# Performance work log

Hardware: AMD Instinct MI355X
Metric: run time of the kernel (lower is better)

Reference implementation:

```python
import jax, jax.numpy as jnp
import numpy as np

B, T_DEC, U, T_K, D, V = 32, 64, 32, 64, 512, 50257


def setup_inputs() -> dict:
    key = jax.random.key(0)
    ks = jax.random.split(key, 24)
    s = 0.02  # weight init scale
    inp = {
        "target_features": jax.random.normal(ks[0], (B, T_DEC, D), jnp.float32),
        "target_mask": jnp.ones((B, T_DEC), jnp.float32),
        "encode_features": jax.random.normal(ks[1], (B, U, D), jnp.float32),
        "utterance_mask": jnp.ones((B, U), jnp.float32),
        "token_features": jax.random.normal(ks[2], (U, B, T_K, D), jnp.float32),
        "token_mask": jnp.ones((U, B, T_K), jnp.float32),
        "coverage": jnp.zeros((B, U), jnp.float32),
        "token_coverage": jnp.zeros((U, B, T_K), jnp.float32),
        # utterance_attention params
        "ua_Wp": jax.random.normal(ks[3], (D, D), jnp.float32) * s,
        "ua_bp": jnp.zeros((D,), jnp.float32),
        "ua_v": jax.random.normal(ks[4], (D,), jnp.float32) * s,
        "ua_wc": jax.random.normal(ks[5], (D,), jnp.float32) * s,  # W_c: Linear(1,D) weight, squeezed
        # token_attention params
        "ta_Wp": jax.random.normal(ks[6], (D, D), jnp.float32) * s,
        "ta_bp": jnp.zeros((D,), jnp.float32),
        "ta_v": jax.random.normal(ks[7], (D,), jnp.float32) * s,
        "ta_wc": jax.random.normal(ks[8], (D,), jnp.float32) * s,
        # pointer-gen + output projections
        "pgen_W": jax.random.normal(ks[9], (1, 2 * D), jnp.float32) * s,
        "pgen_b": jnp.zeros((1,), jnp.float32),
        "out1_W": jax.random.normal(ks[10], (D, 2 * D), jnp.float32) * s,
        "out1_b": jnp.zeros((D,), jnp.float32),
        "out2_W": jax.random.normal(ks[11], (V, D), jnp.float32) * s,
        "out2_b": jnp.zeros((V,), jnp.float32),
        # LayerNorm params
        "ln_g": jnp.ones((D,), jnp.float32),
        "ln_b": jnp.zeros((D,), jnp.float32),
    }
    return inp


def _local_attn(t, enc, mask, cov, Wp, bp, v, wc):
    # t: [..., D] decoder state, enc: [..., T, D], mask/cov: [..., T]
    dec = t @ Wp.T + bp                                   # [..., D]
    att = enc + dec[..., None, :] + cov[..., None] * wc   # additive + coverage feature
    scores = jnp.einsum('...td,d->...t', jnp.tanh(att), v)
    attn_ = jax.nn.softmax(scores, axis=-1) * mask
    nf = attn_.sum(-1, keepdims=True)
    attn = attn_ / jnp.where(nf == 0, 1.0, nf)
    out = jnp.einsum('...t,...td->...d', attn, enc)       # context vector
    return out, attn, cov + attn


def reference(target_features, target_mask, encode_features, utterance_mask,
              token_features, token_mask, coverage, token_coverage,
              ua_Wp, ua_bp, ua_v, ua_wc, ta_Wp, ta_bp, ta_v, ta_wc,
              pgen_W, pgen_b, out1_W, out1_b, out2_W, out2_b, ln_g, ln_b):
    # layers == [] so the transformer-layer loop is a no-op; then LayerNorm.
    mu = target_features.mean(-1, keepdims=True)
    var = ((target_features - mu) ** 2).mean(-1, keepdims=True)
    normed = (target_features - mu) * jax.lax.rsqrt(var + 1e-5) * ln_g + ln_b
    local_dec = normed[:, -1, :]                           # [B, D]

    # utterance-level attention
    u_out, u_attn, u_cov = _local_attn(local_dec, encode_features, utterance_mask,
                                       coverage, ua_Wp, ua_bp, ua_v, ua_wc)

    # per-utterance token attention, batched over U (replaces Python for-loop)
    tok = jax.vmap(lambda e, m, c: _local_attn(local_dec, e, m, c, ta_Wp, ta_bp, ta_v, ta_wc))
    utters_out, utters_attn, next_tok_cov = tok(token_features, token_mask, token_coverage)
    # utters_out: [U, B, D], utters_attn/next_tok_cov: [U, B, T_K]

    p_gen = jax.nn.sigmoid(jnp.concatenate([u_out, local_dec], axis=1) @ pgen_W.T + pgen_b)

    # topk(k=1) == argmax (first max on ties, matching torch.topk)
    utter_index = jnp.argmax(u_attn, axis=1)               # [B]
    idx = jnp.arange(u_attn.shape[0])
    target_attn_dist = utters_attn[utter_index, idx, :]    # [B, T_K]
    target_out = utters_out[utter_index, idx, :]           # [B, D]

    h = jnp.concatenate([target_out, local_dec], axis=1) @ out1_W.T + out1_b
    logits = h @ out2_W.T + out2_b
    vocab_dist = jax.nn.softmax(logits, axis=1)
    return vocab_dist, target_attn_dist, p_gen, u_cov, next_tok_cov, utter_index
```

## Files before the change

### kernel.cpp

```cpp
#include <hip/hip_runtime.h>
#include <math.h>

#define BB 32
#define TDEC 64
#define UU 32
#define TK 64
#define DD 512
#define VV 50257
#define NT5 3142
#define K5_GRID 1024

#define WS_LDEC   0
#define WS_DEC_U  16384
#define WS_DEC_T  32768
#define WS_UATTN  49152
#define WS_UIDX   50176
#define WS_TSC    50208
#define WS_TATTN  115744
#define WS_TOUT   181280
#define WS_H      197664
#define WS_PSUM   214048
#define WS_SUMS   246816

#define OUT_VOCAB 0
#define OUT_TAD   1608224
#define OUT_PGEN  1610272
#define OUT_UCOV  1610304
#define OUT_NTC   1611328
#define OUT_UIDX  1676864

__device__ __forceinline__ float wave_sum(float v) {
    #pragma unroll
    for (int off = 32; off > 0; off >>= 1) v += __shfl_xor(v, off, 64);
    return v;
}
__device__ __forceinline__ float wave_max(float v) {
    #pragma unroll
    for (int off = 32; off > 0; off >>= 1) v = fmaxf(v, __shfl_xor(v, off, 64));
    return v;
}
__device__ __forceinline__ float fast_tanh(float x) {
    float e2 = __expf(2.0f * x);
    return 1.0f - 2.0f * __builtin_amdgcn_rcpf(e2 + 1.0f);
}

__global__ __launch_bounds__(256) void k1_ln_proj(
    const float* __restrict__ tf, const float* __restrict__ ln_g, const float* __restrict__ ln_b,
    const float* __restrict__ ua_Wp, const float* __restrict__ ua_bp,
    const float* __restrict__ ta_Wp, const float* __restrict__ ta_bp,
    float* __restrict__ ws)
{
    int b = blockIdx.x >> 3, slice = blockIdx.x & 7;
    int tid = threadIdx.x, wid = tid >> 6, lane = tid & 63;
    __shared__ __align__(16) float ldec[DD];
    __shared__ float red[4];
    const float* x = tf + ((size_t)b * TDEC + (TDEC - 1)) * DD;
    float x0 = x[tid], x1 = x[tid + 256];

    float s = wave_sum(x0 + x1);
    if (lane == 0) red[wid] = s;
    __syncthreads();
    float mean = (red[0] + red[1] + red[2] + red[3]) * (1.0f / DD);
    __syncthreads();
    float d0 = x0 - mean, d1 = x1 - mean;
    s = wave_sum(d0 * d0 + d1 * d1);
    if (lane == 0) red[wid] = s;
    __syncthreads();
    float var = (red[0] + red[1] + red[2] + red[3]) * (1.0f / DD);
    float inv = rsqrtf(var + 1e-5f);
    float n0 = d0 * inv * ln_g[tid] + ln_b[tid];
    float n1 = d1 * inv * ln_g[tid + 256] + ln_b[tid + 256];
    ldec[tid] = n0; ldec[tid + 256] = n1;
    if (slice == 0) {
        ws[WS_LDEC + b * DD + tid] = n0;
        ws[WS_LDEC + b * DD + tid + 256] = n1;
    }
    __syncthreads();

    int r = slice * 128 + (tid >> 1);
    int m = r >> 9, rr = r & 511;
    int kh = tid & 1;
    const float* Wp = m ? ta_Wp : ua_Wp;
    const float* bp = m ? ta_bp : ua_bp;
    const float4* wr = (const float4*)(Wp + (size_t)rr * DD + kh * 256);
    const float4* hl = (const float4*)ldec + kh * 64;
    float acc = 0.f;
    #pragma unroll 8
    for (int i = 0; i < 64; i++) {
        float4 w = wr[i]; float4 h = hl[i];
        acc += w.x * h.x + w.y * h.y + w.z * h.z + w.w * h.w;
    }
    float tot = acc + __shfl_xor(acc, 1, 64);
    if (kh == 0) {
        float* dst = ws + (m ? WS_DEC_T : WS_DEC_U) + b * DD + rr;
        *dst = tot + bp[rr];
    }
}

__global__ __launch_bounds__(256) void k2_uattn(
    const float* __restrict__ enc, const float* __restrict__ umask,
    const float* __restrict__ cov, const float* __restrict__ ua_v,
    const float* __restrict__ ua_wc, const float* __restrict__ pgen_W,
    const float* __restrict__ pgen_b,
    float* __restrict__ ws, float* __restrict__ out)
{
    int b = blockIdx.x, tid = threadIdx.x, wid = tid >> 6, lane = tid & 63;
    __shared__ __align__(16) float decu[DD], wcl[DD], vvl[DD], ldec[DD], uo[DD];
    __shared__ float sc[UU], attn[UU], red[4];
    decu[tid] = ws[WS_DEC_U + b * DD + tid]; decu[tid + 256] = ws[WS_DEC_U + b * DD + tid + 256];
    wcl[tid] = ua_wc[tid]; wcl[tid + 256] = ua_wc[tid + 256];
    vvl[tid] = ua_v[tid];  vvl[tid + 256] = ua_v[tid + 256];
    ldec[tid] = ws[WS_LDEC + b * DD + tid]; ldec[tid + 256] = ws[WS_LDEC + b * DD + tid + 256];
    __syncthreads();

    for (int u = wid; u < UU; u += 4) {
        float cb = cov[b * UU + u];
        const float* e = enc + ((size_t)b * UU + u) * DD;
        float p = 0.f;
        #pragma unroll
        for (int i = 0; i < DD / 64; i++) {
            int d = lane + i * 64;
            p += fast_tanh(e[d] + decu[d] + cb * wcl[d]) * vvl[d];
        }
        p = wave_sum(p);
        if (lane == 0) sc[u] = p;
    }
    __syncthreads();

    if (tid < 64) {
        float s = (tid < UU) ? sc[tid] : -INFINITY;
        float m = wave_max(s);
        float e = (tid < UU) ? __expf(s - m) : 0.f;
        float sum = wave_sum(e);
        float a_ = (e / sum) * ((tid < UU) ? umask[b * UU + tid] : 0.f);
        float nf = wave_sum(a_);
        float a = a_ / (nf == 0.f ? 1.f : nf);
        float av = (tid < UU) ? a : -INFINITY;
        float am = wave_max(av);
        unsigned long long ball = __ballot(av == am);
        int idx = __ffsll(ball) - 1;
        if (tid < UU) {
            attn[tid] = a;
            ws[WS_UATTN + b * UU + tid] = a;
            out[OUT_UCOV + b * UU + tid] = cov[b * UU + tid] + a;
        }
        if (tid == 0) {
            ((int*)ws)[WS_UIDX + b] = idx;
            out[OUT_UIDX + b] = (float)idx;
        }
    }
    __syncthreads();

    for (int d = tid; d < DD; d += 256) {
        float s = 0.f;
        #pragma unroll
        for (int u = 0; u < UU; u++) s += attn[u] * enc[((size_t)b * UU + u) * DD + d];
        uo[d] = s;
    }
    __syncthreads();

    float pp = uo[tid] * pgen_W[tid] + uo[tid + 256] * pgen_W[tid + 256]
             + ldec[tid] * pgen_W[DD + tid] + ldec[tid + 256] * pgen_W[DD + tid + 256];
    pp = wave_sum(pp);
    if (lane == 0) red[wid] = pp;
    __syncthreads();
    if (tid == 0) {
        float t = red[0] + red[1] + red[2] + red[3] + pgen_b[0];
        out[OUT_PGEN + b] = 1.f / (1.f + __expf(-t));
    }
}

__global__ __launch_bounds__(256, 4) void k3a_tscore(
    const float* __restrict__ tok, const float* __restrict__ tcov,
    const float* __restrict__ ta_v, const float* __restrict__ ta_wc,
    float* __restrict__ ws)
{
    int blk = blockIdx.x;
    int u = blk >> 6, r = blk & 63, b = r >> 1, hf = r & 1;
    int tid = threadIdx.x, wid = tid >> 6, lane = tid & 63;

    const float4* dec4 = (const float4*)(ws + WS_DEC_T + b * DD);
    const float4* wc4  = (const float4*)ta_wc;
    const float4* vv4  = (const float4*)ta_v;
    float4 dc0 = dec4[lane], dc1 = dec4[lane + 64];
    float4 wc0 = wc4[lane],  wc1 = wc4[lane + 64];
    float4 vv0 = vv4[lane],  vv1 = vv4[lane + 64];

    const float* base = tok + ((size_t)(u * BB + b)) * TK * DD;
    const float* tcb  = tcov + (size_t)(u * BB + b) * TK;
    int t0 = hf * 32 + wid * 8;

    float4 x[8][2];
    float tc[8];
    #pragma unroll
    for (int j = 0; j < 8; j++) {
        const float4* row = (const float4*)(base + (size_t)(t0 + j) * DD);
        x[j][0] = row[lane];
        x[j][1] = row[lane + 64];
        tc[j] = tcb[t0 + j];
    }
    #pragma unroll
    for (int j = 0; j < 8; j++) {
        float p = 0.f;
        float4 a = x[j][0], c = x[j][1];
        float t_ = tc[j];
        p += fast_tanh(a.x + dc0.x + t_ * wc0.x) * vv0.x;
        p += fast_tanh(a.y + dc0.y + t_ * wc0.y) * vv0.y;
        p += fast_tanh(a.z + dc0.z + t_ * wc0.z) * vv0.z;
        p += fast_tanh(a.w + dc0.w + t_ * wc0.w) * vv0.w;
        p += fast_tanh(c.x + dc1.x + t_ * wc1.x) * vv1.x;
        p += fast_tanh(c.y + dc1.y + t_ * wc1.y) * vv1.y;
        p += fast_tanh(c.z + dc1.z + t_ * wc1.z) * vv1.z;
        p += fast_tanh(c.w + dc1.w + t_ * wc1.w) * vv1.w;
        p = wave_sum(p);
        if (lane == 0) ws[WS_TSC + (size_t)(u * BB + b) * TK + t0 + j] = p;
    }
}

__global__ __launch_bounds__(256) void k3b_tsoftmax(
    const float* __restrict__ tmask, const float* __restrict__ tcov,
    float* __restrict__ ws, float* __restrict__ out)
{
    int tid = threadIdx.x, wid = tid >> 6, lane = tid & 63;
    int g = blockIdx.x * 4 + wid;
    float s = ws[WS_TSC + (size_t)g * TK + lane];
    float m = wave_max(s);
    float e = __expf(s - m);
    float sum = wave_sum(e);
    float a_ = (e / sum) * tmask[(size_t)g * TK + lane];
    float nf = wave_sum(a_);
    float a = a_ / (nf == 0.f ? 1.f : nf);
    ws[WS_TATTN + (size_t)g * TK + lane] = a;
    out[OUT_NTC + (size_t)g * TK + lane] = tcov[(size_t)g * TK + lane] + a;
}

__global__ __launch_bounds__(256) void k4a_gather(
    const float* __restrict__ tok, float* __restrict__ ws, float* __restrict__ out)
{
    int b = blockIdx.x, tid = threadIdx.x;
    __shared__ float at[TK];
    int u = ((const int*)ws)[WS_UIDX + b];
    if (tid < TK) {
        float a = ws[WS_TATTN + (size_t)(u * BB + b) * TK + tid];
        at[tid] = a;
        out[OUT_TAD + b * TK + tid] = a;
    }
    __syncthreads();
    const float* base = tok + ((size_t)(u * BB + b)) * TK * DD;
    float a0 = 0.f, a1 = 0.f;
    #pragma unroll 8
    for (int t = 0; t < TK; t++) {
        float a = at[t];
        a0 += a * base[(size_t)t * DD + tid];
        a1 += a * base[(size_t)t * DD + tid + 256];
    }
    ws[WS_TOUT + b * DD + tid] = a0;
    ws[WS_TOUT + b * DD + tid + 256] = a1;
}

__global__ __launch_bounds__(256) void k4b_h(
    const float* __restrict__ out1_W, const float* __restrict__ out1_b,
    float* __restrict__ ws)
{
    int slice = blockIdx.x >> 5, b = blockIdx.x & 31;
    int tid = threadIdx.x;
    __shared__ __align__(16) float hcat[2 * DD];
    hcat[tid]       = ws[WS_TOUT + b * DD + tid];
    hcat[tid + 256] = ws[WS_TOUT + b * DD + tid + 256];
    hcat[tid + 512] = ws[WS_LDEC + b * DD + tid];
    hcat[tid + 768] = ws[WS_LDEC + b * DD + tid + 256];
    __syncthreads();

    int row = slice * 128 + (tid >> 1);
    int kh = tid & 1;
    const float4* wr = (const float4*)(out1_W + (size_t)row * (2 * DD) + kh * 512);
    const float4* hl = (const float4*)hcat + kh * 128;
    float acc = 0.f;
    #pragma unroll 8
    for (int i = 0; i < 128; i++) {
        float4 w = wr[i]; float4 h = hl[i];
        acc += w.x * h.x + w.y * h.y + w.z * h.z + w.w * h.w;
    }
    float tot = acc + __shfl_xor(acc, 1, 64);
    if (kh == 0) ws[WS_H + b * DD + row] = tot + out1_b[row];
}

__global__ __launch_bounds__(512, 4) void k5_gemv(
    const float* __restrict__ W2, const float* __restrict__ b2,
    float* __restrict__ ws, float* __restrict__ out)
{
    int tid = threadIdx.x;
    int b = tid & 31, kc = tid >> 5;
    __shared__ float red[16 * 16 * 33];
    float4 hr[8];
    {
        const float4* hp = (const float4*)(ws + WS_H + b * DD + kc * 32);
        #pragma unroll
        for (int i = 0; i < 8; i++) hr[i] = hp[i];
    }
    int jj = tid & 15, bb = tid >> 4;
    float es = 0.f;

    for (int tile = blockIdx.x; tile < NT5; tile += K5_GRID) {
        int v0 = tile * 16;
        float acc[16];
        #pragma unroll
        for (int j = 0; j < 16; j++) acc[j] = 0.f;
        #pragma unroll 2
        for (int j = 0; j < 16; j++) {
            int v = v0 + j;
            if (v < VV) {
                const float4* wr = (const float4*)(W2 + (size_t)v * DD + kc * 32);
                float a = 0.f;
                #pragma unroll
                for (int i = 0; i < 8; i++) {
                    float4 w = wr[i];
                    a += w.x * hr[i].x + w.y * hr[i].y + w.z * hr[i].z + w.w * hr[i].w;
                }
                acc[j] = a;
            }
        }
        #pragma unroll
        for (int j = 0; j < 16; j++) red[(kc * 16 + j) * 33 + b] = acc[j];
        __syncthreads();
        {
            int v = v0 + jj;
            if (v < VV) {
                float s = 0.f;
                #pragma unroll
                for (int k = 0; k < 16; k++) s += red[(k * 16 + jj) * 33 + bb];
                float e = __expf(s + b2[v]);
                out[(size_t)bb * VV + v] = e;
                es += e;
            }
        }
        __syncthreads();
    }
    #pragma unroll
    for (int off = 1; off < 16; off <<= 1) es += __shfl_xor(es, off, 64);
    if (jj == 0) ws[WS_PSUM + blockIdx.x * 32 + bb] = es;
}

__global__ __launch_bounds__(256) void k_sum(float* __restrict__ ws)
{
    int tid = threadIdx.x;
    int b = tid & 31, c = tid >> 5;
    __shared__ float red8[8][32];
    float p = 0.f;
    for (int g = c * 128; g < (c + 1) * 128; g++) p += ws[WS_PSUM + g * 32 + b];
    red8[c][b] = p;
    __syncthreads();
    if (tid < 32) {
        float s = 0.f;
        #pragma unroll
        for (int c2 = 0; c2 < 8; c2++) s += red8[c2][tid];
        ws[WS_SUMS + tid] = 1.0f / s;
    }
}

__global__ __launch_bounds__(256) void k_scale(const float* __restrict__ ws, float* __restrict__ out)
{
    int b = blockIdx.y;
    int v = blockIdx.x * 256 + threadIdx.x;
    if (v < VV) out[(size_t)b * VV + v] *= ws[WS_SUMS + b];
}

extern "C" void kernel_launch(void* const* d_in, const int* in_sizes, int n_in,
                              void* d_out, int out_size, void* d_ws, size_t ws_size,
                              hipStream_t stream) {
    const float* tf      = (const float*)d_in[0];
    const float* enc     = (const float*)d_in[2];
    const float* umask   = (const float*)d_in[3];
    const float* tok     = (const float*)d_in[4];
    const float* tmask   = (const float*)d_in[5];
    const float* cov     = (const float*)d_in[6];
    const float* tcov    = (const float*)d_in[7];
    const float* ua_Wp   = (const float*)d_in[8];
    const float* ua_bp   = (const float*)d_in[9];
    const float* ua_v    = (const float*)d_in[10];
    const float* ua_wc   = (const float*)d_in[11];
    const float* ta_Wp   = (const float*)d_in[12];
    const float* ta_bp   = (const float*)d_in[13];
    const float* ta_v    = (const float*)d_in[14];
    const float* ta_wc   = (const float*)d_in[15];
    const float* pgen_W  = (const float*)d_in[16];
    const float* pgen_b  = (const float*)d_in[17];
    const float* out1_W  = (const float*)d_in[18];
    const float* out1_b  = (const float*)d_in[19];
    const float* out2_W  = (const float*)d_in[20];
    const float* out2_b  = (const float*)d_in[21];
    const float* ln_g    = (const float*)d_in[22];
    const float* ln_b    = (const float*)d_in[23];

    float* ws  = (float*)d_ws;
    float* out = (float*)d_out;

    k1_ln_proj<<<dim3(256), dim3(256), 0, stream>>>(tf, ln_g, ln_b, ua_Wp, ua_bp, ta_Wp, ta_bp, ws);
    k2_uattn<<<dim3(BB), dim3(256), 0, stream>>>(enc, umask, cov, ua_v, ua_wc, pgen_W, pgen_b, ws, out);
    k3a_tscore<<<dim3(2048), dim3(256), 0, stream>>>(tok, tcov, ta_v, ta_wc, ws);
    k3b_tsoftmax<<<dim3(256), dim3(256), 0, stream>>>(tmask, tcov, ws, out);
    k4a_gather<<<dim3(BB), dim3(256), 0, stream>>>(tok, ws, out);
    k4b_h<<<dim3(128), dim3(256), 0, stream>>>(out1_W, out1_b, ws);
    k5_gemv<<<dim3(K5_GRID), dim3(512), 0, stream>>>(out2_W, out2_b, ws, out);
    k_sum<<<dim3(1), dim3(256), 0, stream>>>(ws);
    k_scale<<<dim3(197, 32), dim3(256), 0, stream>>>(ws, out);
}
```

Baseline: 475.4 us.

## Replace vocab GEMV with shared-memory tiled GEMM using register blocking

```diff
diff --git a/kernel.cpp b/kernel.cpp
--- a/kernel.cpp
+++ b/kernel.cpp
@@ -7,8 +7,8 @@
 #define TK 64
 #define DD 512
 #define VV 50257
-#define NT5 3142
-#define K5_GRID 1024
+#define N5TILE 256
+#define K5_GRID 197
 
 #define WS_LDEC   0
 #define WS_DEC_U  16384
@@ -285,60 +285,97 @@
     if (kh == 0) ws[WS_H + b * DD + row] = tot + out1_b[row];
 }
 
-__global__ __launch_bounds__(512, 4) void k5_gemv(
+__global__ __launch_bounds__(256) void k5_gemm(
     const float* __restrict__ W2, const float* __restrict__ b2,
     float* __restrict__ ws, float* __restrict__ out)
 {
+    __shared__ __align__(16) float W2t[32 * 260];
+    __shared__ __align__(16) float htl[32 * 36];
+    __shared__ float pr[32 * 33];
+
     int tid = threadIdx.x;
-    int b = tid & 31, kc = tid >> 5;
-    __shared__ float red[16 * 16 * 33];
-    float4 hr[8];
-    {
-        const float4* hp = (const float4*)(ws + WS_H + b * DD + kc * 32);
-        #pragma unroll
-        for (int i = 0; i < 8; i++) hr[i] = hp[i];
-    }
-    int jj = tid & 15, bb = tid >> 4;
-    float es = 0.f;
-
-    for (int tile = blockIdx.x; tile < NT5; tile += K5_GRID) {
-        int v0 = tile * 16;
-        float acc[16];
-        #pragma unroll
-        for (int j = 0; j < 16; j++) acc[j] = 0.f;
-        #pragma unroll 2
-        for (int j = 0; j < 16; j++) {
-            int v = v0 + j;
-            if (v < VV) {
-                const float4* wr = (const float4*)(W2 + (size_t)v * DD + kc * 32);
-                float a = 0.f;
-                #pragma unroll
-                for (int i = 0; i < 8; i++) {
-                    float4 w = wr[i];
-                    a += w.x * hr[i].x + w.y * hr[i].y + w.z * hr[i].z + w.w * hr[i].w;
-                }
-                acc[j] = a;
-            }
-        }
-        #pragma unroll
-        for (int j = 0; j < 16; j++) red[(kc * 16 + j) * 33 + b] = acc[j];
+    int bg = tid >> 5;
+    int vg = tid & 31;
+    int b0 = bg * 4;
+    int vg8 = vg * 8;
+    int v0base = blockIdx.x * N5TILE;
+
+    int kq = (tid & 7) * 4;
+    int sr = tid >> 3;
+
+    float acc[4][8];
+    #pragma unroll
+    for (int i = 0; i < 4; i++)
+        #pragma unroll
+        for (int j = 0; j < 8; j++) acc[i][j] = 0.f;
+
+    for (int kt = 0; kt < 16; kt++) {
+        int k0 = kt * 32;
+        {
+            float4 hv = *(const float4*)(ws + WS_H + sr * DD + k0 + kq);
+            htl[(kq + 0) * 36 + sr] = hv.x;
+            htl[(kq + 1) * 36 + sr] = hv.y;
+            htl[(kq + 2) * 36 + sr] = hv.z;
+            htl[(kq + 3) * 36 + sr] = hv.w;
+        }
+        #pragma unroll
+        for (int p = 0; p < 8; p++) {
+            int lv = p * 32 + sr;
+            int v = v0base + lv;
+            float4 wv = {0.f, 0.f, 0.f, 0.f};
+            if (v < VV) wv = *(const float4*)(W2 + (size_t)v * DD + k0 + kq);
+            W2t[(kq + 0) * 260 + lv] = wv.x;
+            W2t[(kq + 1) * 260 + lv] = wv.y;
+            W2t[(kq + 2) * 260 + lv] = wv.z;
+            W2t[(kq + 3) * 260 + lv] = wv.w;
+        }
         __syncthreads();
-        {
-            int v = v0 + jj;
-            if (v < VV) {
-                float s = 0.f;
-                #pragma unroll
-                for (int k = 0; k < 16; k++) s += red[(k * 16 + jj) * 33 + bb];
-                float e = __expf(s + b2[v]);
-                out[(size_t)bb * VV + v] = e;
+        #pragma unroll 4
+        for (int k = 0; k < 32; k++) {
+            float4 hb = *(const float4*)&htl[k * 36 + b0];
+            float4 wa = *(const float4*)&W2t[k * 260 + vg8];
+            float4 wb = *(const float4*)&W2t[k * 260 + vg8 + 4];
+            acc[0][0] += hb.x * wa.x; acc[0][1] += hb.x * wa.y; acc[0][2] += hb.x * wa.z; acc[0][3] += hb.x * wa.w;
+            acc[0][4] += hb.x * wb.x; acc[0][5] += hb.x * wb.y; acc[0][6] += hb.x * wb.z; acc[0][7] += hb.x * wb.w;
+            acc[1][0] += hb.y * wa.x; acc[1][1] += hb.y * wa.y; acc[1][2] += hb.y * wa.z; acc[1][3] += hb.y * wa.w;
+            acc[1][4] += hb.y * wb.x; acc[1][5] += hb.y * wb.y; acc[1][6] += hb.y * wb.z; acc[1][7] += hb.y * wb.w;
+            acc[2][0] += hb.z * wa.x; acc[2][1] += hb.z * wa.y; acc[2][2] += hb.z * wa.z; acc[2][3] += hb.z * wa.w;
+            acc[2][4] += hb.z * wb.x; acc[2][5] += hb.z * wb.y; acc[2][6] += hb.z * wb.z; acc[2][7] += hb.z * wb.w;
+            acc[3][0] += hb.w * wa.x; acc[3][1] += hb.w * wa.y; acc[3][2] += hb.w * wa.z; acc[3][3] += hb.w * wa.w;
+            acc[3][4] += hb.w * wb.x; acc[3][5] += hb.w * wb.y; acc[3][6] += hb.w * wb.z; acc[3][7] += hb.w * wb.w;
+        }
+        __syncthreads();
+    }
+
+    int v0 = v0base + vg8;
+    float b2v[8];
+    #pragma unroll
+    for (int vi = 0; vi < 8; vi++) b2v[vi] = (v0 + vi < VV) ? b2[v0 + vi] : 0.f;
+
+    float esum[4];
+    #pragma unroll
+    for (int bi = 0; bi < 4; bi++) {
+        float es = 0.f;
+        float* op = out + (size_t)(b0 + bi) * VV + v0;
+        #pragma unroll
+        for (int vi = 0; vi < 8; vi++) {
+            if (v0 + vi < VV) {
+                float e = __expf(acc[bi][vi] + b2v[vi]);
+                op[vi] = e;
                 es += e;
             }
         }
-        __syncthreads();
-    }
-    #pragma unroll
-    for (int off = 1; off < 16; off <<= 1) es += __shfl_xor(es, off, 64);
-    if (jj == 0) ws[WS_PSUM + blockIdx.x * 32 + bb] = es;
+        esum[bi] = es;
+    }
+    #pragma unroll
+    for (int bi = 0; bi < 4; bi++) pr[(b0 + bi) * 33 + vg] = esum[bi];
+    __syncthreads();
+    if (tid < 32) {
+        float s = 0.f;
+        #pragma unroll 8
+        for (int j = 0; j < 32; j++) s += pr[tid * 33 + j];
+        ws[WS_PSUM + blockIdx.x * 32 + tid] = s;
+    }
 }
 
 __global__ __launch_bounds__(256) void k_sum(float* __restrict__ ws)
@@ -347,7 +384,9 @@
     int b = tid & 31, c = tid >> 5;
     __shared__ float red8[8][32];
     float p = 0.f;
-    for (int g = c * 128; g < (c + 1) * 128; g++) p += ws[WS_PSUM + g * 32 + b];
+    int g0 = c * 25, g1 = (c + 1) * 25;
+    if (g1 > K5_GRID) g1 = K5_GRID;
+    for (int g = g0; g < g1; g++) p += ws[WS_PSUM + g * 32 + b];
     red8[c][b] = p;
     __syncthreads();
     if (tid < 32) {
@@ -401,7 +440,7 @@
     k3b_tsoftmax<<<dim3(256), dim3(256), 0, stream>>>(tmask, tcov, ws, out);
     k4a_gather<<<dim3(BB), dim3(256), 0, stream>>>(tok, ws, out);
     k4b_h<<<dim3(128), dim3(256), 0, stream>>>(out1_W, out1_b, ws);
-    k5_gemv<<<dim3(K5_GRID), dim3(512), 0, stream>>>(out2_W, out2_b, ws, out);
+    k5_gemm<<<dim3(K5_GRID), dim3(256), 0, stream>>>(out2_W, out2_b, ws, out);
     k_sum<<<dim3(1), dim3(256), 0, stream>>>(ws);
     k_scale<<<dim3(197, 32), dim3(256), 0, stream>>>(ws, out);
 }
```

Result: faster. 458.2 us (-3.6%).
